# Optimization experiments

Hardware: AMD Instinct MI355X
Metric: run time of the kernel (lower is better)

Reference implementation:

```python
import jax, jax.numpy as jnp
import numpy as np

IN_DIM = 1024
HID = 1024


def setup_inputs() -> dict:
    key = jax.random.key(0)
    ks = jax.random.split(key, 20)
    u = lambda k, shape: jax.random.uniform(k, shape, jnp.float32, -0.1, 0.1)
    inp = {
        "x": jax.random.normal(ks[0], (32, 512, IN_DIM), jnp.float32),
        "h0": jnp.zeros((1, 32, HID), jnp.float32),
        "c0": jnp.zeros((1, 32, HID), jnp.float32),
        "W_ii": u(ks[1], (IN_DIM, HID)), "W_if": u(ks[2], (IN_DIM, HID)),
        "W_ig": u(ks[3], (IN_DIM, HID)), "W_io": u(ks[4], (IN_DIM, HID)),
        "W_hi": u(ks[5], (HID, HID)), "W_hf": u(ks[6], (HID, HID)),
        "W_hg": u(ks[7], (HID, HID)), "W_ho": u(ks[8], (HID, HID)),
        "b_ii": u(ks[9], (HID,)), "b_if": u(ks[10], (HID,)),
        "b_ig": u(ks[11], (HID,)), "b_io": u(ks[12], (HID,)),
        "b_hi": u(ks[13], (HID,)), "b_hf": u(ks[14], (HID,)),
        "b_hg": u(ks[15], (HID,)), "b_ho": u(ks[16], (HID,)),
    }
    return inp


def _lstm(x, h0, c0, W_ii, W_if, W_ig, W_io, W_hi, W_hf, W_hg, W_ho,
          b_ii, b_if, b_ig, b_io, b_hi, b_hf, b_hg, b_ho):
    # Precompute all input projections in one big GEMM per gate: [B,S,H]
    xi = jnp.einsum('bsd,dh->bsh', x, W_ii) + b_ii + b_hi
    xf = jnp.einsum('bsd,dh->bsh', x, W_if) + b_if + b_hf
    xg = jnp.einsum('bsd,dh->bsh', x, W_ig) + b_ig + b_hg
    xo = jnp.einsum('bsd,dh->bsh', x, W_io) + b_io + b_ho
    # stack over time for scan: [S, B, H]
    xs = (jnp.swapaxes(xi, 0, 1), jnp.swapaxes(xf, 0, 1),
          jnp.swapaxes(xg, 0, 1), jnp.swapaxes(xo, 0, 1))

    def step(carry, xt):
        h, c = carry
        xti, xtf, xtg, xto = xt
        i = jax.nn.sigmoid(xti + h @ W_hi)
        f = jax.nn.sigmoid(xtf + h @ W_hf)
        g = jnp.tanh(xtg + h @ W_hg)
        o = jax.nn.sigmoid(xto + h @ W_ho)
        c = f * c + i * g
        h = o * jnp.tanh(c)
        return (h, c), h

    (ht, ct), ys = jax.lax.scan(step, (h0[0], c0[0]), xs)
    output = jnp.swapaxes(ys, 0, 1)  # [B, S, H]
    return output, (ht, ct)


def reference(x, h0, c0, W_ii, W_if, W_ig, W_io, W_hi, W_hf, W_hg, W_ho,
              b_ii, b_if, b_ig, b_io, b_hi, b_hf, b_hg, b_ho):
    return _lstm(x, h0, c0, W_ii, W_if, W_ig, W_io, W_hi, W_hf, W_hg, W_ho,
                 b_ii, b_if, b_ig, b_io, b_hi, b_hf, b_hg, b_ho)
```

## Files before the change

kernel.cpp:

```cpp
#include <hip/hip_runtime.h>
#include <cstdint>
#include <cstddef>

typedef __attribute__((ext_vector_type(8))) short s16x8;
typedef __attribute__((ext_vector_type(4))) short s16x4;
typedef __attribute__((ext_vector_type(4))) float f32x4;
typedef unsigned long long u64;

#define HID 1024
#define BATCH 32
#define SEQ 512
#define NWG 128

__device__ __forceinline__ short f2bf(float f){
  unsigned u = __builtin_bit_cast(unsigned, f);
  u = (u + 0x7fffu + ((u >> 16) & 1u)) >> 16;
  return (short)u;
}
__device__ __forceinline__ float bf2f(short s){
  unsigned u = ((unsigned)(unsigned short)s) << 16;
  return __builtin_bit_cast(float, u);
}

union U128 { struct { u64 lo, hi; } q; s16x8 v; };

__global__ __launch_bounds__(256) void pack_x_kernel(const float* __restrict__ x,
                                                     s16x8* __restrict__ xpk){
  int P = blockIdx.x * 256 + threadIdx.x;
  int lane = P & 63;
  int w = (P >> 6) & 15; int ks = w >> 3, mt = w & 7;
  int tile = P >> 10; int kt = tile & 15; int mb = tile >> 4;
  int row = mb * 128 + mt * 16 + (lane & 15);
  int k0 = kt * 64 + ks * 32 + (lane >> 4) * 8;
  const f32x4* src = (const f32x4*)(x + (size_t)row * HID + k0);
  f32x4 v0 = src[0], v1 = src[1];
  s16x8 o;
  o[0]=f2bf(v0[0]); o[1]=f2bf(v0[1]); o[2]=f2bf(v0[2]); o[3]=f2bf(v0[3]);
  o[4]=f2bf(v1[0]); o[5]=f2bf(v1[1]); o[6]=f2bf(v1[2]); o[7]=f2bf(v1[3]);
  xpk[P] = o;
}

__global__ __launch_bounds__(256) void pack_wx_kernel(const float* __restrict__ Wii,
    const float* __restrict__ Wif, const float* __restrict__ Wig,
    const float* __restrict__ Wio, s16x8* __restrict__ wxpk){
  int P = blockIdx.x * 256 + threadIdx.x;
  int lane = P & 63;
  int w = (P >> 6) & 15; int ks = w >> 3, nt = w & 7;
  int tile = P >> 10; int kt = tile & 15; int nb = tile >> 4;
  int n = nb * 128 + nt * 16 + (lane & 15);
  int g = n >> 10, c = n & 1023;
  int k0 = kt * 64 + ks * 32 + (lane >> 4) * 8;
  const float* W = (g == 0) ? Wii : (g == 1) ? Wif : (g == 2) ? Wig : Wio;
  s16x8 o;
  #pragma unroll
  for (int j = 0; j < 8; ++j) o[j] = f2bf(W[(size_t)(k0 + j) * HID + c]);
  wxpk[P] = o;
}

__global__ __launch_bounds__(256) void pack_wh_kernel(const float* __restrict__ Whi,
    const float* __restrict__ Whf, const float* __restrict__ Whg,
    const float* __restrict__ Who, s16x8* __restrict__ whpk){
  int P = blockIdx.x * 256 + threadIdx.x;
  int lane = P & 63;
  int q = P >> 6;
  int nt = q & 1; int ks = (q >> 1) & 1; int kt = (q >> 2) & 15; int wg = q >> 6;
  int col16 = lane & 15;
  int g = nt * 2 + (col16 >> 3);
  int c = wg * 8 + (col16 & 7);
  int k0 = kt * 64 + ks * 32 + (lane >> 4) * 8;
  const float* W = (g == 0) ? Whi : (g == 1) ? Whf : (g == 2) ? Whg : Who;
  s16x8 o;
  #pragma unroll
  for (int j = 0; j < 8; ++j) o[j] = f2bf(W[(size_t)(k0 + j) * HID + c]);
  whpk[P] = o;
}

__global__ __launch_bounds__(256) void init_kernel(const float* __restrict__ h0,
    const float* bii, const float* bif, const float* big, const float* bio,
    const float* bhi, const float* bhf, const float* bhg, const float* bho,
    float* __restrict__ bias_sum, u64* __restrict__ hseq, int* __restrict__ flags){
  int T = blockIdx.x * 256 + threadIdx.x;
  if (T < 4096){
    int g = T >> 10, c = T & 1023;
    const float* bi = (g == 0) ? bii : (g == 1) ? bif : (g == 2) ? big : bio;
    const float* bh = (g == 0) ? bhi : (g == 1) ? bhf : (g == 2) ? bhg : bho;
    bias_sum[T] = bi[c] + bh[c];
  } else if (T < 8192){
    int u = T - 4096;
    int lane = u & 63; int q = u >> 6;
    int kstep = q & 31; int mtb = q >> 5;
    int b = mtb * 16 + (lane & 15);
    int col0 = kstep * 32 + (lane >> 4) * 8;
    const float* src = h0 + (size_t)b * HID + col0;
    s16x8 o;
    #pragma unroll
    for (int j = 0; j < 8; ++j) o[j] = f2bf(src[j]);
    u64 lo = (u64)(unsigned short)o[0] | ((u64)(unsigned short)o[1]<<16)
           | ((u64)(unsigned short)o[2]<<32) | ((u64)(unsigned short)o[3]<<48);
    u64 hi = (u64)(unsigned short)o[4] | ((u64)(unsigned short)o[5]<<16)
           | ((u64)(unsigned short)o[6]<<32) | ((u64)(unsigned short)o[7]<<48);
    __hip_atomic_store(hseq + 2*u,     lo, __ATOMIC_RELAXED, __HIP_MEMORY_SCOPE_AGENT);
    __hip_atomic_store(hseq + 2*u + 1, hi, __ATOMIC_RELAXED, __HIP_MEMORY_SCOPE_AGENT);
  } else if (T < 8192 + SEQ * NWG){
    flags[T - 8192] = 0;
  }
}

__global__ __launch_bounds__(256) void gemm_xp_kernel(const s16x8* __restrict__ xpk,
    const s16x8* __restrict__ wxpk, const float* __restrict__ bias_sum,
    short* __restrict__ XP){
  const int mb = blockIdx.x, nb = blockIdx.y;
  const int tid = threadIdx.x, lane = tid & 63, wave = tid >> 6;
  const int wr = wave >> 1, wc = wave & 1;
  __shared__ s16x8 sA[1024];
  __shared__ s16x8 sB[1024];
  f32x4 acc[4][4] = {};
  const s16x8* gA = xpk + (size_t)(mb * 16) * 1024;
  const s16x8* gB = wxpk + (size_t)(nb * 16) * 1024;
  for (int kt = 0; kt < 16; ++kt){
    __syncthreads();
    #pragma unroll
    for (int i = 0; i < 4; ++i){
      sA[i * 256 + tid] = gA[(size_t)kt * 1024 + i * 256 + tid];
      sB[i * 256 + tid] = gB[(size_t)kt * 1024 + i * 256 + tid];
    }
    __syncthreads();
    #pragma unroll
    for (int ks = 0; ks < 2; ++ks){
      s16x8 af[4], bfr[4];
      #pragma unroll
      for (int i = 0; i < 4; ++i) af[i] = sA[(ks * 8 + wr * 4 + i) * 64 + lane];
      #pragma unroll
      for (int j = 0; j < 4; ++j) bfr[j] = sB[(ks * 8 + wc * 4 + j) * 64 + lane];
      #pragma unroll
      for (int i = 0; i < 4; ++i)
        #pragma unroll
        for (int j = 0; j < 4; ++j)
          acc[i][j] = __builtin_amdgcn_mfma_f32_16x16x32_bf16(af[i], bfr[j], acc[i][j], 0, 0, 0);
    }
  }
  #pragma unroll
  for (int i = 0; i < 4; ++i){
    const int m_base = mb * 128 + (wr * 4 + i) * 16 + ((lane >> 4) << 2);
    #pragma unroll
    for (int j = 0; j < 4; ++j){
      const int n = nb * 128 + (wc * 4 + j) * 16 + (lane & 15);
      const float bias = bias_sum[n];
      const int g = n >> 10, c = n & 1023;
      #pragma unroll
      for (int r = 0; r < 4; ++r){
        const int m = m_base + r;
        const int tt = m & 511, bb = m >> 9;
        XP[(((size_t)(tt * 32 + bb) << 10) + c) * 4 + g] = f2bf(acc[i][j][r] + bias);
      }
    }
  }
}

__global__ __launch_bounds__(256, 1) void lstm_rec_kernel(const s16x8* __restrict__ whpk,
    u64* __restrict__ hseq, int* __restrict__ flags, const short* __restrict__ XP,
    const float* __restrict__ c0, float* __restrict__ out, float* __restrict__ htct)
{
  extern __shared__ char smem[];
  s16x8* sW  = (s16x8*)smem;
  float* pre = (float*)(smem + 65536);
  unsigned short* hstage = (unsigned short*)(smem + 65536 + 4224);

  const int wg = blockIdx.x;
  const int tid = threadIdx.x, lane = tid & 63, wave = tid >> 6;
  const int mt = wave >> 1, nt = wave & 1;

  {
    const s16x8* gW = whpk + (size_t)wg * 4096;
    #pragma unroll
    for (int i = 0; i < 16; ++i) sW[i * 256 + tid] = gW[i * 256 + tid];
  }

  const int b = tid >> 3, cc = tid & 7;
  const int hcol = wg * 8 + cc;
  float c = c0[b * HID + hcol];

  const int prow = mt * 16 + ((lane >> 4) << 2);
  const int pcol = nt * 16 + (lane & 15);

  const int pub_off = (tid >> 5) * 4096 + (wg >> 2) * 128 + (wg & 3) * 32 + (tid & 31);

  s16x4 xp = *(const s16x4*)(XP + ((((size_t)b) << 10) + hcol) * 4);

  __syncthreads();

  for (int t = 0; t < SEQ; ++t){
    if (t > 0){
      const u64* fp = (const u64*)(flags + (size_t)t * NWG) + lane;
      while (true){
        u64 v = __hip_atomic_load(fp, __ATOMIC_RELAXED, __HIP_MEMORY_SCOPE_AGENT);
        if (__all(v == 0x0000000100000001ull)) break;
        __builtin_amdgcn_s_sleep(1);
      }
    }
    const u64* h_cur = hseq + (size_t)(t & 3) * 8192;

    f32x4 a0 = {0.f,0.f,0.f,0.f}, a1 = a0, a2 = a0, a3 = a0;
    #pragma unroll
    for (int kk = 0; kk < 8; ++kk){
      U128 h0f, h1f, h2f, h3f;
      {
        int u = (mt * 32 + 0 * 8 + kk) * 64 + lane;
        h0f.q.lo = __hip_atomic_load(h_cur + 2*u,   __ATOMIC_RELAXED, __HIP_MEMORY_SCOPE_AGENT);
        h0f.q.hi = __hip_atomic_load(h_cur + 2*u+1, __ATOMIC_RELAXED, __HIP_MEMORY_SCOPE_AGENT);
      }
      {
        int u = (mt * 32 + 1 * 8 + kk) * 64 + lane;
        h1f.q.lo = __hip_atomic_load(h_cur + 2*u,   __ATOMIC_RELAXED, __HIP_MEMORY_SCOPE_AGENT);
        h1f.q.hi = __hip_atomic_load(h_cur + 2*u+1, __ATOMIC_RELAXED, __HIP_MEMORY_SCOPE_AGENT);
      }
      {
        int u = (mt * 32 + 2 * 8 + kk) * 64 + lane;
        h2f.q.lo = __hip_atomic_load(h_cur + 2*u,   __ATOMIC_RELAXED, __HIP_MEMORY_SCOPE_AGENT);
        h2f.q.hi = __hip_atomic_load(h_cur + 2*u+1, __ATOMIC_RELAXED, __HIP_MEMORY_SCOPE_AGENT);
      }
      {
        int u = (mt * 32 + 3 * 8 + kk) * 64 + lane;
        h3f.q.lo = __hip_atomic_load(h_cur + 2*u,   __ATOMIC_RELAXED, __HIP_MEMORY_SCOPE_AGENT);
        h3f.q.hi = __hip_atomic_load(h_cur + 2*u+1, __ATOMIC_RELAXED, __HIP_MEMORY_SCOPE_AGENT);
      }
      a0 = __builtin_amdgcn_mfma_f32_16x16x32_bf16(h0f.v, sW[((0*8+kk)*2+nt)*64+lane], a0, 0, 0, 0);
      a1 = __builtin_amdgcn_mfma_f32_16x16x32_bf16(h1f.v, sW[((1*8+kk)*2+nt)*64+lane], a1, 0, 0, 0);
      a2 = __builtin_amdgcn_mfma_f32_16x16x32_bf16(h2f.v, sW[((2*8+kk)*2+nt)*64+lane], a2, 0, 0, 0);
      a3 = __builtin_amdgcn_mfma_f32_16x16x32_bf16(h3f.v, sW[((3*8+kk)*2+nt)*64+lane], a3, 0, 0, 0);
    }
    f32x4 acc = (a0 + a1) + (a2 + a3);

    pre[(prow + 0) * 33 + pcol] = acc[0];
    pre[(prow + 1) * 33 + pcol] = acc[1];
    pre[(prow + 2) * 33 + pcol] = acc[2];
    pre[(prow + 3) * 33 + pcol] = acc[3];
    __syncthreads();

    float p0 = pre[b * 33 + 0 * 8 + cc] + bf2f(xp[0]);
    float p1 = pre[b * 33 + 1 * 8 + cc] + bf2f(xp[1]);
    float p2 = pre[b * 33 + 2 * 8 + cc] + bf2f(xp[2]);
    float p3 = pre[b * 33 + 3 * 8 + cc] + bf2f(xp[3]);
    float ig = 1.f / (1.f + __expf(-p0));
    float fg = 1.f / (1.f + __expf(-p1));
    float gg = tanhf(p2);
    float og = 1.f / (1.f + __expf(-p3));
    c = fg * c + ig * gg;
    float h = og * tanhf(c);
    out[((size_t)b * SEQ + t) * HID + hcol] = h;
    if (t == SEQ - 1){
      htct[b * HID + hcol] = h;
      htct[32 * HID + b * HID + hcol] = c;
      break;
    }
    hstage[(t & 1) * 256 + b * 8 + cc] = (unsigned short)f2bf(h);

    const int tn = t + 1;
    s16x4 xp_n = *(const s16x4*)(XP + ((((size_t)tn * 32 + b) << 10) + hcol) * 4);

    __syncthreads();

    if (tid < 64){
      u64 val = ((const u64*)(hstage + (t & 1) * 256))[tid];
      __hip_atomic_store(hseq + (size_t)((t + 1) & 3) * 8192 + pub_off, val,
                         __ATOMIC_RELAXED, __HIP_MEMORY_SCOPE_AGENT);
    }
    if (tid == 0){
      asm volatile("s_waitcnt vmcnt(0)" ::: "memory");
      __hip_atomic_store(&flags[(size_t)(t + 1) * NWG + wg], 1,
                         __ATOMIC_RELAXED, __HIP_MEMORY_SCOPE_AGENT);
    }
    xp = xp_n;
  }
}

extern "C" void kernel_launch(void* const* d_in, const int* in_sizes, int n_in,
                              void* d_out, int out_size, void* d_ws, size_t ws_size,
                              hipStream_t stream){
  const float* x   = (const float*)d_in[0];
  const float* h0  = (const float*)d_in[1];
  const float* c0  = (const float*)d_in[2];
  const float* Wii = (const float*)d_in[3];
  const float* Wif = (const float*)d_in[4];
  const float* Wig = (const float*)d_in[5];
  const float* Wio = (const float*)d_in[6];
  const float* Whi = (const float*)d_in[7];
  const float* Whf = (const float*)d_in[8];
  const float* Whg = (const float*)d_in[9];
  const float* Who = (const float*)d_in[10];
  const float* bii = (const float*)d_in[11];
  const float* bif = (const float*)d_in[12];
  const float* big = (const float*)d_in[13];
  const float* bio = (const float*)d_in[14];
  const float* bhi = (const float*)d_in[15];
  const float* bhf = (const float*)d_in[16];
  const float* bhg = (const float*)d_in[17];
  const float* bho = (const float*)d_in[18];

  char* ws = (char*)d_ws;
  s16x8* xpk      = (s16x8*)(ws);
  s16x8* wxpk     = (s16x8*)(ws + 33554432ull);
  s16x8* whpk     = (s16x8*)(ws + 41943040ull);
  short* XP       = (short*)(ws + 50331648ull);
  u64*   hseq     = (u64*)  (ws + 184549376ull);
  float* bias_sum = (float*)(ws + 184811520ull);
  int*   flags    = (int*)  (ws + 184827904ull);

  float* out  = (float*)d_out;
  float* htct = out + (size_t)BATCH * SEQ * HID;

  pack_x_kernel<<<8192, 256, 0, stream>>>(x, xpk);
  pack_wx_kernel<<<2048, 256, 0, stream>>>(Wii, Wif, Wig, Wio, wxpk);
  pack_wh_kernel<<<2048, 256, 0, stream>>>(Whi, Whf, Whg, Who, whpk);
  init_kernel<<<288, 256, 0, stream>>>(h0, bii, bif, big, bio,
                                       bhi, bhf, bhg, bho, bias_sum, hseq, flags);
  gemm_xp_kernel<<<dim3(128, 32), 256, 0, stream>>>(xpk, wxpk, bias_sum, XP);

  void* args[] = {(void*)&whpk, (void*)&hseq, (void*)&flags, (void*)&XP,
                  (void*)&c0, (void*)&out, (void*)&htct};
  hipLaunchCooperativeKernel((const void*)lstm_rec_kernel, dim3(NWG), dim3(256),
                             args, 65536 + 4224 + 1024, stream);
}
```

Baseline: 3.556 ms.

## Halve recurrent workgroups and sync per-wave with transposed MFMA layout

Rewrites the persistent LSTM recurrence to use 64 workgroups, each holding 16 hidden columns (128KB of W_h in LDS). The MFMA is transposed so each wave produces gate pre-activations for its own batch half directly in registers. This removes the LDS staging and both __syncthreads per timestep. Each wave publishes its h values and a per-wave 16-bit flag, and consumers poll only the flags for their batch half, so the barrier is finer-grained. In exchange each step does more MFMA work per workgroup, holds 32 h fragments in registers, and uses more LDS, with fewer CUs doing the recurrence.

```diff
diff --git a/kernel.cpp b/kernel.cpp
--- a/kernel.cpp
+++ b/kernel.cpp
@@ -3,14 +3,13 @@
 #include <cstddef>
 
 typedef __attribute__((ext_vector_type(8))) short s16x8;
-typedef __attribute__((ext_vector_type(4))) short s16x4;
 typedef __attribute__((ext_vector_type(4))) float f32x4;
 typedef unsigned long long u64;
 
 #define HID 1024
 #define BATCH 32
 #define SEQ 512
-#define NWG 128
+#define NWG 64
 
 __device__ __forceinline__ short f2bf(float f){
   unsigned u = __builtin_bit_cast(unsigned, f);
@@ -62,12 +61,13 @@
     const float* __restrict__ Who, s16x8* __restrict__ whpk){
   int P = blockIdx.x * 256 + threadIdx.x;
   int lane = P & 63;
-  int q = P >> 6;
-  int nt = q & 1; int ks = (q >> 1) & 1; int kt = (q >> 2) & 15; int wg = q >> 6;
-  int col16 = lane & 15;
-  int g = nt * 2 + (col16 >> 3);
-  int c = wg * 8 + (col16 & 7);
-  int k0 = kt * 64 + ks * 32 + (lane >> 4) * 8;
+  int mt = (P >> 6) & 3;
+  int q  = (P >> 8) & 31;
+  int wg = P >> 13;
+  int m16 = lane & 15;
+  int g = m16 & 3;
+  int c = wg * 16 + mt * 4 + (m16 >> 2);
+  int k0 = q * 32 + (lane >> 4) * 8;
   const float* W = (g == 0) ? Whi : (g == 1) ? Whf : (g == 2) ? Whg : Who;
   s16x8 o;
   #pragma unroll
@@ -101,7 +101,7 @@
            | ((u64)(unsigned short)o[6]<<32) | ((u64)(unsigned short)o[7]<<48);
     __hip_atomic_store(hseq + 2*u,     lo, __ATOMIC_RELAXED, __HIP_MEMORY_SCOPE_AGENT);
     __hip_atomic_store(hseq + 2*u + 1, hi, __ATOMIC_RELAXED, __HIP_MEMORY_SCOPE_AGENT);
-  } else if (T < 8192 + SEQ * NWG){
+  } else if (T < 8192 + 65536){
     flags[T - 8192] = 0;
   }
 }
@@ -151,126 +151,123 @@
       for (int r = 0; r < 4; ++r){
         const int m = m_base + r;
         const int tt = m & 511, bb = m >> 9;
-        XP[(((size_t)(tt * 32 + bb) << 10) + c) * 4 + g] = f2bf(acc[i][j][r] + bias);
+        XP[(((size_t)tt * 1024 + c) * 32 + bb) * 4 + g] = f2bf(acc[i][j][r] + bias);
       }
     }
   }
 }
 
 __global__ __launch_bounds__(256, 1) void lstm_rec_kernel(const s16x8* __restrict__ whpk,
-    u64* __restrict__ hseq, int* __restrict__ flags, const short* __restrict__ XP,
-    const float* __restrict__ c0, float* __restrict__ out, float* __restrict__ htct)
+    u64* __restrict__ hseq, unsigned short* __restrict__ flags,
+    const short* __restrict__ XP, const float* __restrict__ c0,
+    float* __restrict__ out, float* __restrict__ htct)
 {
   extern __shared__ char smem[];
-  s16x8* sW  = (s16x8*)smem;
-  float* pre = (float*)(smem + 65536);
-  unsigned short* hstage = (unsigned short*)(smem + 65536 + 4224);
+  s16x8* sW = (s16x8*)smem;
 
   const int wg = blockIdx.x;
   const int tid = threadIdx.x, lane = tid & 63, wave = tid >> 6;
-  const int mt = wave >> 1, nt = wave & 1;
+  const int mp = wave >> 1, nt = wave & 1;
 
   {
-    const s16x8* gW = whpk + (size_t)wg * 4096;
-    #pragma unroll
-    for (int i = 0; i < 16; ++i) sW[i * 256 + tid] = gW[i * 256 + tid];
-  }
-
-  const int b = tid >> 3, cc = tid & 7;
-  const int hcol = wg * 8 + cc;
-  float c = c0[b * HID + hcol];
-
-  const int prow = mt * 16 + ((lane >> 4) << 2);
-  const int pcol = nt * 16 + (lane & 15);
-
-  const int pub_off = (tid >> 5) * 4096 + (wg >> 2) * 128 + (wg & 3) * 32 + (tid & 31);
-
-  s16x4 xp = *(const s16x4*)(XP + ((((size_t)b) << 10) + hcol) * 4);
+    const s16x8* gW = whpk + (size_t)wg * 8192;
+    #pragma unroll
+    for (int i = 0; i < 32; ++i) sW[i * 256 + tid] = gW[i * 256 + tid];
+  }
+
+  const int l16 = lane & 15, lhi = lane >> 4;
+  const int b = nt * 16 + l16;
+  const int hc0 = wg * 16 + mp * 8 + lhi;
+  const int hc1 = hc0 + 4;
+  float cst0 = c0[b * HID + hc0];
+  float cst1 = c0[b * HID + hc1];
+
+  const int pub0 = (((nt * 32 + (hc0 >> 5)) * 64 + ((hc0 >> 3) & 3) * 16 + l16) << 3) + (hc0 & 7);
+  const int pub1 = (((nt * 32 + (hc1 >> 5)) * 64 + ((hc1 >> 3) & 3) * 16 + l16) << 3) + (hc1 & 7);
 
   __syncthreads();
+
+  const u64* XPq = (const u64*)XP;
+  u64 xq0 = XPq[(size_t)hc0 * 32 + b];
+  u64 xq1 = XPq[(size_t)hc1 * 32 + b];
+
+  const int a0base = mp * 2, a1base = mp * 2 + 1;
 
   for (int t = 0; t < SEQ; ++t){
     if (t > 0){
-      const u64* fp = (const u64*)(flags + (size_t)t * NWG) + lane;
+      const u64* fp = (const u64*)(flags + (size_t)t * 256 + nt * 128) + (lane & 31);
       while (true){
         u64 v = __hip_atomic_load(fp, __ATOMIC_RELAXED, __HIP_MEMORY_SCOPE_AGENT);
-        if (__all(v == 0x0000000100000001ull)) break;
+        if (__all(v == 0x0001000100010001ull)) break;
         __builtin_amdgcn_s_sleep(1);
       }
     }
-    const u64* h_cur = hseq + (size_t)(t & 3) * 8192;
-
-    f32x4 a0 = {0.f,0.f,0.f,0.f}, a1 = a0, a2 = a0, a3 = a0;
-    #pragma unroll
-    for (int kk = 0; kk < 8; ++kk){
-      U128 h0f, h1f, h2f, h3f;
-      {
-        int u = (mt * 32 + 0 * 8 + kk) * 64 + lane;
-        h0f.q.lo = __hip_atomic_load(h_cur + 2*u,   __ATOMIC_RELAXED, __HIP_MEMORY_SCOPE_AGENT);
-        h0f.q.hi = __hip_atomic_load(h_cur + 2*u+1, __ATOMIC_RELAXED, __HIP_MEMORY_SCOPE_AGENT);
-      }
-      {
-        int u = (mt * 32 + 1 * 8 + kk) * 64 + lane;
-        h1f.q.lo = __hip_atomic_load(h_cur + 2*u,   __ATOMIC_RELAXED, __HIP_MEMORY_SCOPE_AGENT);
-        h1f.q.hi = __hip_atomic_load(h_cur + 2*u+1, __ATOMIC_RELAXED, __HIP_MEMORY_SCOPE_AGENT);
-      }
-      {
-        int u = (mt * 32 + 2 * 8 + kk) * 64 + lane;
-        h2f.q.lo = __hip_atomic_load(h_cur + 2*u,   __ATOMIC_RELAXED, __HIP_MEMORY_SCOPE_AGENT);
-        h2f.q.hi = __hip_atomic_load(h_cur + 2*u+1, __ATOMIC_RELAXED, __HIP_MEMORY_SCOPE_AGENT);
-      }
-      {
-        int u = (mt * 32 + 3 * 8 + kk) * 64 + lane;
-        h3f.q.lo = __hip_atomic_load(h_cur + 2*u,   __ATOMIC_RELAXED, __HIP_MEMORY_SCOPE_AGENT);
-        h3f.q.hi = __hip_atomic_load(h_cur + 2*u+1, __ATOMIC_RELAXED, __HIP_MEMORY_SCOPE_AGENT);
-      }
-      a0 = __builtin_amdgcn_mfma_f32_16x16x32_bf16(h0f.v, sW[((0*8+kk)*2+nt)*64+lane], a0, 0, 0, 0);
-      a1 = __builtin_amdgcn_mfma_f32_16x16x32_bf16(h1f.v, sW[((1*8+kk)*2+nt)*64+lane], a1, 0, 0, 0);
-      a2 = __builtin_amdgcn_mfma_f32_16x16x32_bf16(h2f.v, sW[((2*8+kk)*2+nt)*64+lane], a2, 0, 0, 0);
-      a3 = __builtin_amdgcn_mfma_f32_16x16x32_bf16(h3f.v, sW[((3*8+kk)*2+nt)*64+lane], a3, 0, 0, 0);
-    }
-    f32x4 acc = (a0 + a1) + (a2 + a3);
-
-    pre[(prow + 0) * 33 + pcol] = acc[0];
-    pre[(prow + 1) * 33 + pcol] = acc[1];
-    pre[(prow + 2) * 33 + pcol] = acc[2];
-    pre[(prow + 3) * 33 + pcol] = acc[3];
-    __syncthreads();
-
-    float p0 = pre[b * 33 + 0 * 8 + cc] + bf2f(xp[0]);
-    float p1 = pre[b * 33 + 1 * 8 + cc] + bf2f(xp[1]);
-    float p2 = pre[b * 33 + 2 * 8 + cc] + bf2f(xp[2]);
-    float p3 = pre[b * 33 + 3 * 8 + cc] + bf2f(xp[3]);
-    float ig = 1.f / (1.f + __expf(-p0));
-    float fg = 1.f / (1.f + __expf(-p1));
-    float gg = tanhf(p2);
-    float og = 1.f / (1.f + __expf(-p3));
-    c = fg * c + ig * gg;
-    float h = og * tanhf(c);
-    out[((size_t)b * SEQ + t) * HID + hcol] = h;
+    const u64* hs = hseq + (size_t)(t & 3) * 8192;
+
+    U128 hb[32];
+    #pragma unroll
+    for (int q = 0; q < 32; ++q){
+      const int u = (nt * 32 + q) * 64 + lane;
+      hb[q].q.lo = __hip_atomic_load(hs + 2 * u,     __ATOMIC_RELAXED, __HIP_MEMORY_SCOPE_AGENT);
+      hb[q].q.hi = __hip_atomic_load(hs + 2 * u + 1, __ATOMIC_RELAXED, __HIP_MEMORY_SCOPE_AGENT);
+    }
+
+    f32x4 a00 = {0.f,0.f,0.f,0.f}, a01 = a00, a10 = a00, a11 = a00;
+    #pragma unroll
+    for (int q = 0; q < 32; q += 2){
+      a00 = __builtin_amdgcn_mfma_f32_16x16x32_bf16(sW[(q * 4 + a0base) * 64 + lane],       hb[q].v,     a00, 0, 0, 0);
+      a10 = __builtin_amdgcn_mfma_f32_16x16x32_bf16(sW[(q * 4 + a1base) * 64 + lane],       hb[q].v,     a10, 0, 0, 0);
+      a01 = __builtin_amdgcn_mfma_f32_16x16x32_bf16(sW[((q + 1) * 4 + a0base) * 64 + lane], hb[q + 1].v, a01, 0, 0, 0);
+      a11 = __builtin_amdgcn_mfma_f32_16x16x32_bf16(sW[((q + 1) * 4 + a1base) * 64 + lane], hb[q + 1].v, a11, 0, 0, 0);
+    }
+    f32x4 p0 = a00 + a01;
+    f32x4 p1 = a10 + a11;
+
+    float pi0 = p0[0] + bf2f((short)(xq0 & 0xffff));
+    float pf0 = p0[1] + bf2f((short)((xq0 >> 16) & 0xffff));
+    float pg0 = p0[2] + bf2f((short)((xq0 >> 32) & 0xffff));
+    float po0 = p0[3] + bf2f((short)(xq0 >> 48));
+    float pi1 = p1[0] + bf2f((short)(xq1 & 0xffff));
+    float pf1 = p1[1] + bf2f((short)((xq1 >> 16) & 0xffff));
+    float pg1 = p1[2] + bf2f((short)((xq1 >> 32) & 0xffff));
+    float po1 = p1[3] + bf2f((short)(xq1 >> 48));
+
+    float ig0 = 1.f / (1.f + __expf(-pi0));
+    float fg0 = 1.f / (1.f + __expf(-pf0));
+    float gg0 = tanhf(pg0);
+    float og0 = 1.f / (1.f + __expf(-po0));
+    float ig1 = 1.f / (1.f + __expf(-pi1));
+    float fg1 = 1.f / (1.f + __expf(-pf1));
+    float gg1 = tanhf(pg1);
+    float og1 = 1.f / (1.f + __expf(-po1));
+
+    cst0 = fg0 * cst0 + ig0 * gg0;
+    cst1 = fg1 * cst1 + ig1 * gg1;
+    float h0v = og0 * tanhf(cst0);
+    float h1v = og1 * tanhf(cst1);
+
     if (t == SEQ - 1){
-      htct[b * HID + hcol] = h;
-      htct[32 * HID + b * HID + hcol] = c;
+      out[((size_t)b * SEQ + t) * HID + hc0] = h0v;
+      out[((size_t)b * SEQ + t) * HID + hc1] = h1v;
+      htct[b * HID + hc0] = h0v;
+      htct[b * HID + hc1] = h1v;
+      htct[32 * HID + b * HID + hc0] = cst0;
+      htct[32 * HID + b * HID + hc1] = cst1;
       break;
     }
-    hstage[(t & 1) * 256 + b * 8 + cc] = (unsigned short)f2bf(h);
-
-    const int tn = t + 1;
-    s16x4 xp_n = *(const s16x4*)(XP + ((((size_t)tn * 32 + b) << 10) + hcol) * 4);
-
-    __syncthreads();
-
-    if (tid < 64){
-      u64 val = ((const u64*)(hstage + (t & 1) * 256))[tid];
-      __hip_atomic_store(hseq + (size_t)((t + 1) & 3) * 8192 + pub_off, val,
-                         __ATOMIC_RELAXED, __HIP_MEMORY_SCOPE_AGENT);
-    }
-    if (tid == 0){
-      asm volatile("s_waitcnt vmcnt(0)" ::: "memory");
-      __hip_atomic_store(&flags[(size_t)(t + 1) * NWG + wg], 1,
-                         __ATOMIC_RELAXED, __HIP_MEMORY_SCOPE_AGENT);
-    }
-    xp = xp_n;
+
+    unsigned short* hp = (unsigned short*)(hseq + (size_t)((t + 1) & 3) * 8192);
+    __hip_atomic_store(hp + pub0, (unsigned short)f2bf(h0v), __ATOMIC_RELAXED, __HIP_MEMORY_SCOPE_AGENT);
+    __hip_atomic_store(hp + pub1, (unsigned short)f2bf(h1v), __ATOMIC_RELAXED, __HIP_MEMORY_SCOPE_AGENT);
+    asm volatile("s_waitcnt vmcnt(0)" ::: "memory");
+    if (lane == 0)
+      __hip_atomic_store(flags + (size_t)(t + 1) * 256 + nt * 128 + wg * 2 + mp,
+                         (unsigned short)1, __ATOMIC_RELAXED, __HIP_MEMORY_SCOPE_AGENT);
+
+    out[((size_t)b * SEQ + t) * HID + hc0] = h0v;
+    out[((size_t)b * SEQ + t) * HID + hc1] = h1v;
+    xq0 = XPq[((size_t)(t + 1) * 1024 + hc0) * 32 + b];
+    xq1 = XPq[((size_t)(t + 1) * 1024 + hc1) * 32 + b];
   }
 }
 
@@ -319,5 +316,5 @@
   void* args[] = {(void*)&whpk, (void*)&hseq, (void*)&flags, (void*)&XP,
                   (void*)&c0, (void*)&out, (void*)&htct};
   hipLaunchCooperativeKernel((const void*)lstm_rec_kernel, dim3(NWG), dim3(256),
-                             args, 65536 + 4224 + 1024, stream);
-}
+                             args, 131072, stream);
+}
```

Result: slower. 4.327 ms (+21.7%).

## Fuse input-projection GEMM into recurrent kernel with producer/consumer overlap

Applied to the files above, without the earlier changes.

Removes the separate input-projection GEMM launch and instead runs it on 112 extra workgroups inside the cooperative recurrent kernel. The GEMM tiles are reordered so the timesteps are produced in quarters, and each quarter bumps a counter that the recurrent workgroups poll before consuming those timesteps. The step-level sync moves to per-wave flags published via shuffles instead of an LDS staging buffer plus a block barrier, and the output store is deferred until after publishing h. This hides the GEMM behind the serial recurrence and shortens the per-step critical path, at the cost of GEMM blocks competing for memory bandwidth and extra polling traffic.

```diff
diff --git a/kernel.cpp b/kernel.cpp
--- a/kernel.cpp
+++ b/kernel.cpp
@@ -3,14 +3,15 @@
 #include <cstddef>
 
 typedef __attribute__((ext_vector_type(8))) short s16x8;
-typedef __attribute__((ext_vector_type(4))) short s16x4;
 typedef __attribute__((ext_vector_type(4))) float f32x4;
 typedef unsigned long long u64;
 
 #define HID 1024
 #define BATCH 32
 #define SEQ 512
-#define NWG 128
+#define NWG_REC 128
+#define NWG_GEMM 112
+#define NWG_TOT 240
 
 __device__ __forceinline__ short f2bf(float f){
   unsigned u = __builtin_bit_cast(unsigned, f);
@@ -78,7 +79,8 @@
 __global__ __launch_bounds__(256) void init_kernel(const float* __restrict__ h0,
     const float* bii, const float* bif, const float* big, const float* bio,
     const float* bhi, const float* bhf, const float* bhg, const float* bho,
-    float* __restrict__ bias_sum, u64* __restrict__ hseq, int* __restrict__ flags){
+    float* __restrict__ bias_sum, u64* __restrict__ hseq,
+    unsigned int* __restrict__ hflags32, unsigned int* __restrict__ XPflag){
   int T = blockIdx.x * 256 + threadIdx.x;
   if (T < 4096){
     int g = T >> 10, c = T & 1023;
@@ -101,73 +103,88 @@
            | ((u64)(unsigned short)o[6]<<32) | ((u64)(unsigned short)o[7]<<48);
     __hip_atomic_store(hseq + 2*u,     lo, __ATOMIC_RELAXED, __HIP_MEMORY_SCOPE_AGENT);
     __hip_atomic_store(hseq + 2*u + 1, hi, __ATOMIC_RELAXED, __HIP_MEMORY_SCOPE_AGENT);
-  } else if (T < 8192 + SEQ * NWG){
-    flags[T - 8192] = 0;
-  }
-}
-
-__global__ __launch_bounds__(256) void gemm_xp_kernel(const s16x8* __restrict__ xpk,
+  } else if (T < 8192 + 131072){
+    hflags32[T - 8192] = 0;
+  } else if (T < 8192 + 131072 + 128){
+    XPflag[T - 8192 - 131072] = 0;
+  }
+}
+
+__global__ __launch_bounds__(256, 1) void lstm_fused_kernel(
+    const s16x8* __restrict__ whpk, const s16x8* __restrict__ xpk,
     const s16x8* __restrict__ wxpk, const float* __restrict__ bias_sum,
-    short* __restrict__ XP){
-  const int mb = blockIdx.x, nb = blockIdx.y;
-  const int tid = threadIdx.x, lane = tid & 63, wave = tid >> 6;
-  const int wr = wave >> 1, wc = wave & 1;
-  __shared__ s16x8 sA[1024];
-  __shared__ s16x8 sB[1024];
-  f32x4 acc[4][4] = {};
-  const s16x8* gA = xpk + (size_t)(mb * 16) * 1024;
-  const s16x8* gB = wxpk + (size_t)(nb * 16) * 1024;
-  for (int kt = 0; kt < 16; ++kt){
-    __syncthreads();
-    #pragma unroll
-    for (int i = 0; i < 4; ++i){
-      sA[i * 256 + tid] = gA[(size_t)kt * 1024 + i * 256 + tid];
-      sB[i * 256 + tid] = gB[(size_t)kt * 1024 + i * 256 + tid];
-    }
-    __syncthreads();
-    #pragma unroll
-    for (int ks = 0; ks < 2; ++ks){
-      s16x8 af[4], bfr[4];
-      #pragma unroll
-      for (int i = 0; i < 4; ++i) af[i] = sA[(ks * 8 + wr * 4 + i) * 64 + lane];
-      #pragma unroll
-      for (int j = 0; j < 4; ++j) bfr[j] = sB[(ks * 8 + wc * 4 + j) * 64 + lane];
-      #pragma unroll
-      for (int i = 0; i < 4; ++i)
-        #pragma unroll
-        for (int j = 0; j < 4; ++j)
-          acc[i][j] = __builtin_amdgcn_mfma_f32_16x16x32_bf16(af[i], bfr[j], acc[i][j], 0, 0, 0);
-    }
-  }
-  #pragma unroll
-  for (int i = 0; i < 4; ++i){
-    const int m_base = mb * 128 + (wr * 4 + i) * 16 + ((lane >> 4) << 2);
-    #pragma unroll
-    for (int j = 0; j < 4; ++j){
-      const int n = nb * 128 + (wc * 4 + j) * 16 + (lane & 15);
-      const float bias = bias_sum[n];
-      const int g = n >> 10, c = n & 1023;
-      #pragma unroll
-      for (int r = 0; r < 4; ++r){
-        const int m = m_base + r;
-        const int tt = m & 511, bb = m >> 9;
-        XP[(((size_t)(tt * 32 + bb) << 10) + c) * 4 + g] = f2bf(acc[i][j][r] + bias);
-      }
-    }
-  }
-}
-
-__global__ __launch_bounds__(256, 1) void lstm_rec_kernel(const s16x8* __restrict__ whpk,
-    u64* __restrict__ hseq, int* __restrict__ flags, const short* __restrict__ XP,
+    u64* __restrict__ hseq, unsigned short* __restrict__ hflags,
+    unsigned int* __restrict__ XPflag, short* __restrict__ XP,
     const float* __restrict__ c0, float* __restrict__ out, float* __restrict__ htct)
 {
   extern __shared__ char smem[];
+  const int bid = blockIdx.x;
+  const int tid = threadIdx.x, lane = tid & 63, wave = tid >> 6;
+
+  if (bid >= NWG_REC){
+    s16x8* sA = (s16x8*)smem;
+    s16x8* sB = sA + 1024;
+    const int wr = wave >> 1, wc = wave & 1;
+    for (int tau = bid - NWG_REC; tau < 4096; tau += NWG_GEMM){
+      const int mb_lin = tau >> 5;
+      const int mb = ((mb_lin & 31) << 2) | (mb_lin >> 5);
+      const int nb = tau & 31;
+      f32x4 acc[4][4] = {};
+      const s16x8* gA = xpk + (size_t)(mb * 16) * 1024;
+      const s16x8* gB = wxpk + (size_t)(nb * 16) * 1024;
+      for (int kt = 0; kt < 16; ++kt){
+        __syncthreads();
+        #pragma unroll
+        for (int i = 0; i < 4; ++i){
+          sA[i * 256 + tid] = gA[(size_t)kt * 1024 + i * 256 + tid];
+          sB[i * 256 + tid] = gB[(size_t)kt * 1024 + i * 256 + tid];
+        }
+        __syncthreads();
+        #pragma unroll
+        for (int ks = 0; ks < 2; ++ks){
+          s16x8 af[4], bfr[4];
+          #pragma unroll
+          for (int i = 0; i < 4; ++i) af[i] = sA[(ks * 8 + wr * 4 + i) * 64 + lane];
+          #pragma unroll
+          for (int j = 0; j < 4; ++j) bfr[j] = sB[(ks * 8 + wc * 4 + j) * 64 + lane];
+          #pragma unroll
+          for (int i = 0; i < 4; ++i)
+            #pragma unroll
+            for (int j = 0; j < 4; ++j)
+              acc[i][j] = __builtin_amdgcn_mfma_f32_16x16x32_bf16(af[i], bfr[j], acc[i][j], 0, 0, 0);
+        }
+      }
+      unsigned short* XPu = (unsigned short*)XP;
+      #pragma unroll
+      for (int i = 0; i < 4; ++i){
+        const int m_base = mb * 128 + (wr * 4 + i) * 16 + ((lane >> 4) << 2);
+        #pragma unroll
+        for (int j = 0; j < 4; ++j){
+          const int n = nb * 128 + (wc * 4 + j) * 16 + (lane & 15);
+          const float bias = bias_sum[n];
+          const int g = n >> 10, cxl = n & 1023;
+          #pragma unroll
+          for (int r = 0; r < 4; ++r){
+            const int m = m_base + r;
+            const int tt = m & 511, bb = m >> 9;
+            unsigned short v = (unsigned short)f2bf(acc[i][j][r] + bias);
+            __hip_atomic_store(XPu + ((((size_t)(tt * 32 + bb)) << 10) + cxl) * 4 + g,
+                               v, __ATOMIC_RELAXED, __HIP_MEMORY_SCOPE_AGENT);
+          }
+        }
+      }
+      asm volatile("s_waitcnt vmcnt(0)" ::: "memory");
+      __syncthreads();
+      if (tid == 0)
+        __hip_atomic_fetch_add(&XPflag[mb & 3], 1u, __ATOMIC_RELAXED, __HIP_MEMORY_SCOPE_AGENT);
+    }
+    return;
+  }
+
   s16x8* sW  = (s16x8*)smem;
   float* pre = (float*)(smem + 65536);
-  unsigned short* hstage = (unsigned short*)(smem + 65536 + 4224);
-
-  const int wg = blockIdx.x;
-  const int tid = threadIdx.x, lane = tid & 63, wave = tid >> 6;
+
+  const int wg = bid;
   const int mt = wave >> 1, nt = wave & 1;
 
   {
@@ -183,47 +200,50 @@
   const int prow = mt * 16 + ((lane >> 4) << 2);
   const int pcol = nt * 16 + (lane & 15);
 
-  const int pub_off = (tid >> 5) * 4096 + (wg >> 2) * 128 + (wg & 3) * 32 + (tid & 31);
-
-  s16x4 xp = *(const s16x4*)(XP + ((((size_t)b) << 10) + hcol) * 4);
-
+  const int unit = ((b >> 4) * 32 + (wg >> 2)) * 64 + (wg & 3) * 16 + (b & 15);
+  const size_t pubq = (size_t)unit * 2 + ((tid >> 2) & 1);
+  const bool is_asm = ((tid & 3) == 0);
+
+  if (wave == 0){
+    while (__hip_atomic_load(&XPflag[0], __ATOMIC_RELAXED, __HIP_MEMORY_SCOPE_AGENT) < 1024u)
+      __builtin_amdgcn_s_sleep(16);
+  }
   __syncthreads();
 
+  const u64* XPq = (const u64*)XP;
+  u64 xq = __hip_atomic_load(XPq + ((((size_t)b) << 10) + hcol),
+                             __ATOMIC_RELAXED, __HIP_MEMORY_SCOPE_AGENT);
+
   for (int t = 0; t < SEQ; ++t){
-    if (t > 0){
-      const u64* fp = (const u64*)(flags + (size_t)t * NWG) + lane;
+    if (wave == 0 && t > 0){
+      const u64* fp = (const u64*)(hflags + (size_t)t * 512);
       while (true){
-        u64 v = __hip_atomic_load(fp, __ATOMIC_RELAXED, __HIP_MEMORY_SCOPE_AGENT);
-        if (__all(v == 0x0000000100000001ull)) break;
-        __builtin_amdgcn_s_sleep(1);
+        u64 v0 = __hip_atomic_load(fp + lane,      __ATOMIC_RELAXED, __HIP_MEMORY_SCOPE_AGENT);
+        u64 v1 = __hip_atomic_load(fp + 64 + lane, __ATOMIC_RELAXED, __HIP_MEMORY_SCOPE_AGENT);
+        if (__all((v0 == 0x0001000100010001ull) && (v1 == 0x0001000100010001ull))) break;
+        __builtin_amdgcn_s_sleep(2);
       }
     }
-    const u64* h_cur = hseq + (size_t)(t & 3) * 8192;
+    __syncthreads();
+
+    const u64* hs = hseq + (size_t)(t & 3) * 8192;
 
     f32x4 a0 = {0.f,0.f,0.f,0.f}, a1 = a0, a2 = a0, a3 = a0;
     #pragma unroll
     for (int kk = 0; kk < 8; ++kk){
       U128 h0f, h1f, h2f, h3f;
-      {
-        int u = (mt * 32 + 0 * 8 + kk) * 64 + lane;
-        h0f.q.lo = __hip_atomic_load(h_cur + 2*u,   __ATOMIC_RELAXED, __HIP_MEMORY_SCOPE_AGENT);
-        h0f.q.hi = __hip_atomic_load(h_cur + 2*u+1, __ATOMIC_RELAXED, __HIP_MEMORY_SCOPE_AGENT);
-      }
-      {
-        int u = (mt * 32 + 1 * 8 + kk) * 64 + lane;
-        h1f.q.lo = __hip_atomic_load(h_cur + 2*u,   __ATOMIC_RELAXED, __HIP_MEMORY_SCOPE_AGENT);
-        h1f.q.hi = __hip_atomic_load(h_cur + 2*u+1, __ATOMIC_RELAXED, __HIP_MEMORY_SCOPE_AGENT);
-      }
-      {
-        int u = (mt * 32 + 2 * 8 + kk) * 64 + lane;
-        h2f.q.lo = __hip_atomic_load(h_cur + 2*u,   __ATOMIC_RELAXED, __HIP_MEMORY_SCOPE_AGENT);
-        h2f.q.hi = __hip_atomic_load(h_cur + 2*u+1, __ATOMIC_RELAXED, __HIP_MEMORY_SCOPE_AGENT);
-      }
-      {
-        int u = (mt * 32 + 3 * 8 + kk) * 64 + lane;
-        h3f.q.lo = __hip_atomic_load(h_cur + 2*u,   __ATOMIC_RELAXED, __HIP_MEMORY_SCOPE_AGENT);
-        h3f.q.hi = __hip_atomic_load(h_cur + 2*u+1, __ATOMIC_RELAXED, __HIP_MEMORY_SCOPE_AGENT);
-      }
+      { int u = (mt * 32 + 0 * 8 + kk) * 64 + lane;
+        h0f.q.lo = __hip_atomic_load(hs + 2*u,   __ATOMIC_RELAXED, __HIP_MEMORY_SCOPE_AGENT);
+        h0f.q.hi = __hip_atomic_load(hs + 2*u+1, __ATOMIC_RELAXED, __HIP_MEMORY_SCOPE_AGENT); }
+      { int u = (mt * 32 + 1 * 8 + kk) * 64 + lane;
+        h1f.q.lo = __hip_atomic_load(hs + 2*u,   __ATOMIC_RELAXED, __HIP_MEMORY_SCOPE_AGENT);
+        h1f.q.hi = __hip_atomic_load(hs + 2*u+1, __ATOMIC_RELAXED, __HIP_MEMORY_SCOPE_AGENT); }
+      { int u = (mt * 32 + 2 * 8 + kk) * 64 + lane;
+        h2f.q.lo = __hip_atomic_load(hs + 2*u,   __ATOMIC_RELAXED, __HIP_MEMORY_SCOPE_AGENT);
+        h2f.q.hi = __hip_atomic_load(hs + 2*u+1, __ATOMIC_RELAXED, __HIP_MEMORY_SCOPE_AGENT); }
+      { int u = (mt * 32 + 3 * 8 + kk) * 64 + lane;
+        h3f.q.lo = __hip_atomic_load(hs + 2*u,   __ATOMIC_RELAXED, __HIP_MEMORY_SCOPE_AGENT);
+        h3f.q.hi = __hip_atomic_load(hs + 2*u+1, __ATOMIC_RELAXED, __HIP_MEMORY_SCOPE_AGENT); }
       a0 = __builtin_amdgcn_mfma_f32_16x16x32_bf16(h0f.v, sW[((0*8+kk)*2+nt)*64+lane], a0, 0, 0, 0);
       a1 = __builtin_amdgcn_mfma_f32_16x16x32_bf16(h1f.v, sW[((1*8+kk)*2+nt)*64+lane], a1, 0, 0, 0);
       a2 = __builtin_amdgcn_mfma_f32_16x16x32_bf16(h2f.v, sW[((2*8+kk)*2+nt)*64+lane], a2, 0, 0, 0);
@@ -237,40 +257,47 @@
     pre[(prow + 3) * 33 + pcol] = acc[3];
     __syncthreads();
 
-    float p0 = pre[b * 33 + 0 * 8 + cc] + bf2f(xp[0]);
-    float p1 = pre[b * 33 + 1 * 8 + cc] + bf2f(xp[1]);
-    float p2 = pre[b * 33 + 2 * 8 + cc] + bf2f(xp[2]);
-    float p3 = pre[b * 33 + 3 * 8 + cc] + bf2f(xp[3]);
+    float p0 = pre[b * 33 + 0 * 8 + cc] + bf2f((short)(xq & 0xffff));
+    float p1 = pre[b * 33 + 1 * 8 + cc] + bf2f((short)((xq >> 16) & 0xffff));
+    float p2 = pre[b * 33 + 2 * 8 + cc] + bf2f((short)((xq >> 32) & 0xffff));
+    float p3 = pre[b * 33 + 3 * 8 + cc] + bf2f((short)(xq >> 48));
     float ig = 1.f / (1.f + __expf(-p0));
     float fg = 1.f / (1.f + __expf(-p1));
     float gg = tanhf(p2);
     float og = 1.f / (1.f + __expf(-p3));
     c = fg * c + ig * gg;
     float h = og * tanhf(c);
-    out[((size_t)b * SEQ + t) * HID + hcol] = h;
+
     if (t == SEQ - 1){
+      out[((size_t)b * SEQ + t) * HID + hcol] = h;
       htct[b * HID + hcol] = h;
       htct[32 * HID + b * HID + hcol] = c;
       break;
     }
-    hstage[(t & 1) * 256 + b * 8 + cc] = (unsigned short)f2bf(h);
-
+
+    unsigned hu = (unsigned)(unsigned short)f2bf(h);
+    unsigned g0 = __shfl(hu, (lane & 60) | 0);
+    unsigned g1 = __shfl(hu, (lane & 60) | 1);
+    unsigned g2 = __shfl(hu, (lane & 60) | 2);
+    unsigned g3 = __shfl(hu, (lane & 60) | 3);
+    if (is_asm){
+      u64 val = (u64)g0 | ((u64)g1 << 16) | ((u64)g2 << 32) | ((u64)g3 << 48);
+      __hip_atomic_store(hseq + (size_t)((t + 1) & 3) * 8192 + pubq, val,
+                         __ATOMIC_RELAXED, __HIP_MEMORY_SCOPE_AGENT);
+    }
+    asm volatile("s_waitcnt vmcnt(0)" ::: "memory");
+    if (lane == 0)
+      __hip_atomic_store(&hflags[(size_t)(t + 1) * 512 + wg * 4 + wave],
+                         (unsigned short)1, __ATOMIC_RELAXED, __HIP_MEMORY_SCOPE_AGENT);
+
+    out[((size_t)b * SEQ + t) * HID + hcol] = h;
     const int tn = t + 1;
-    s16x4 xp_n = *(const s16x4*)(XP + ((((size_t)tn * 32 + b) << 10) + hcol) * 4);
-
-    __syncthreads();
-
-    if (tid < 64){
-      u64 val = ((const u64*)(hstage + (t & 1) * 256))[tid];
-      __hip_atomic_store(hseq + (size_t)((t + 1) & 3) * 8192 + pub_off, val,
-                         __ATOMIC_RELAXED, __HIP_MEMORY_SCOPE_AGENT);
-    }
-    if (tid == 0){
-      asm volatile("s_waitcnt vmcnt(0)" ::: "memory");
-      __hip_atomic_store(&flags[(size_t)(t + 1) * NWG + wg], 1,
-                         __ATOMIC_RELAXED, __HIP_MEMORY_SCOPE_AGENT);
-    }
-    xp = xp_n;
+    if ((tn & 127) == 0){
+      while (__hip_atomic_load(&XPflag[tn >> 7], __ATOMIC_RELAXED, __HIP_MEMORY_SCOPE_AGENT) < 1024u)
+        __builtin_amdgcn_s_sleep(16);
+    }
+    xq = __hip_atomic_load(XPq + ((((size_t)tn * 32 + b) << 10) + hcol),
+                           __ATOMIC_RELAXED, __HIP_MEMORY_SCOPE_AGENT);
   }
 }
 
@@ -304,7 +331,8 @@
   short* XP       = (short*)(ws + 50331648ull);
   u64*   hseq     = (u64*)  (ws + 184549376ull);
   float* bias_sum = (float*)(ws + 184811520ull);
-  int*   flags    = (int*)  (ws + 184827904ull);
+  unsigned short* hflags = (unsigned short*)(ws + 184827904ull);
+  unsigned int*   XPflag = (unsigned int*)  (ws + 185352192ull);
 
   float* out  = (float*)d_out;
   float* htct = out + (size_t)BATCH * SEQ * HID;
@@ -312,12 +340,13 @@
   pack_x_kernel<<<8192, 256, 0, stream>>>(x, xpk);
   pack_wx_kernel<<<2048, 256, 0, stream>>>(Wii, Wif, Wig, Wio, wxpk);
   pack_wh_kernel<<<2048, 256, 0, stream>>>(Whi, Whf, Whg, Who, whpk);
-  init_kernel<<<288, 256, 0, stream>>>(h0, bii, bif, big, bio,
-                                       bhi, bhf, bhg, bho, bias_sum, hseq, flags);
-  gemm_xp_kernel<<<dim3(128, 32), 256, 0, stream>>>(xpk, wxpk, bias_sum, XP);
-
-  void* args[] = {(void*)&whpk, (void*)&hseq, (void*)&flags, (void*)&XP,
+  init_kernel<<<545, 256, 0, stream>>>(h0, bii, bif, big, bio,
+                                       bhi, bhf, bhg, bho, bias_sum, hseq,
+                                       (unsigned int*)hflags, XPflag);
+
+  void* args[] = {(void*)&whpk, (void*)&xpk, (void*)&wxpk, (void*)&bias_sum,
+                  (void*)&hseq, (void*)&hflags, (void*)&XPflag, (void*)&XP,
                   (void*)&c0, (void*)&out, (void*)&htct};
-  hipLaunchCooperativeKernel((const void*)lstm_rec_kernel, dim3(NWG), dim3(256),
-                             args, 65536 + 4224 + 1024, stream);
-}
+  hipLaunchCooperativeKernel((const void*)lstm_fused_kernel, dim3(NWG_TOT), dim3(256),
+                             args, 65536 + 4224, stream);
+}
```

Measured after the change: 3.356 ms. 1.06x faster.
